# Kernel tuning notes

Measured on AMD Instinct MI355X. Metric: run time of the kernel, lower is better.

The kernel has to match this reference:

```python
import jax, jax.numpy as jnp
import numpy as np

THRESH = 0.1          # affinity threshold from init_kwargs
SCALES = (1, 2, 4, 8, 16)  # dyadic diffusion scales 2^0..2^4


def compute_dist(X):
    # X: [N, d] -> squared-euclidean pairwise distances via Gram matrix
    G = X @ X.T
    dg = jnp.diag(G)
    return dg[None, :] + dg[:, None] - 2.0 * G


def _diffuse(P, F):
    # returns [P^1 F, P^2 F, P^4 F, P^8 F, P^16 F] via 16 sequential applies
    outs = []
    cur = F
    for step in range(1, SCALES[-1] + 1):
        cur = P @ cur
        if step in SCALES:
            outs.append(cur)
    return outs


def _wavelet_bank(P, F):
    # lazy diffusion wavelets: psi_0 = I - P, psi_j = P^{2^{j-1}} - P^{2^j}
    lows = [F] + _diffuse(P, F)            # t = 0,1,2,4,8,16
    psis = [lows[j] - lows[j + 1] for j in range(len(lows) - 1)]  # 5 wavelets
    return psis, lows[-1]                  # (wavelet coeffs, low-pass P^16 F)


def _gwt_features(X):
    # X: [N, d] reweighted point cloud -> [N, 16*d] scattering features
    N, d = X.shape
    W = jnp.exp(-compute_dist(X) / 10.0)
    W = jnp.where(W < THRESH, jnp.zeros_like(W), W)   # sparsify affinity
    deg = W.sum(axis=1, keepdims=True)                # self-loop w=1 => deg>=1
    P = 0.5 * (jnp.eye(N, dtype=X.dtype) + W / deg)   # lazy random walk
    psis, low = _wavelet_bank(P, X)
    firsts = [jnp.abs(p) for p in psis]
    U = jnp.concatenate(firsts, axis=1)               # [N, 5*d] diffuse all at once
    psis2, _ = _wavelet_bank(P, U)
    # second order: |psi_{j2} |psi_{j1} x|| only for j2 > j1 (10 pairs)
    seconds = [jnp.abs(psis2[j2][:, : j2 * d]) for j2 in range(1, len(psis2))]
    return jnp.concatenate([low] + firsts + seconds, axis=1)  # [N, (1+5+10)*d]


def setup_inputs() -> dict:
    key = jax.random.key(0)
    k1, k2 = jax.random.split(key)
    point_clouds = jax.random.normal(k1, (4, 2048, 3), dtype=jnp.float32)
    alphas = jax.random.uniform(k2, (4, 3), dtype=jnp.float32)  # learned param
    return {"point_clouds": point_clouds, "alphas": alphas}


def reference(point_clouds, alphas):
    # point_clouds: [B, N, d]; alphas: [K, d]
    Xb = point_clouds[:, None, :, :] * alphas[None, :, None, :]  # [B, K, N, d]
    feats = jax.vmap(jax.vmap(_gwt_features))(Xb)                # [B, K, N, 16d]
    # per-cloud: cat over K along feature dim then mean over nodes == mean then flatten
    return feats.mean(axis=2).reshape(feats.shape[0], -1)        # [B, K*16*d]
```

## Files before the change

kernel.cpp:

```cpp
#include <hip/hip_runtime.h>
#include <hip/hip_bf16.h>


#define NN 2048
#define NPAIR 16

typedef _Float16 half8 __attribute__((ext_vector_type(8)));
typedef _Float16 f16x2 __attribute__((ext_vector_type(2)));
typedef float f32x4 __attribute__((ext_vector_type(4)));

extern "C" __device__ f16x2 __ocml_exp2_2f16(f16x2);

#define C2F 0.28853900817779268f
#define CWF -0.14426950408889634f
#define NL2T 3.3219280948873623f

template<int MODE>
__global__ __launch_bounds__(512, 8)
void apply_k(const float* __restrict__ pc, const float* __restrict__ alphas,
             float* __restrict__ Xs, _Float16* __restrict__ Xp,
             float* __restrict__ ihd,
             const _Float16* __restrict__ cur, _Float16* __restrict__ out,
             float* __restrict__ lvl, int t,
             const float* __restrict__ LT1u, const float* __restrict__ LT2r,
             float* __restrict__ fout) {
    __shared__ __align__(16) float smem[8576];
    const int tid  = threadIdx.x;
    const int lane = tid & 63;
    const int wv   = tid >> 6;
    const int p    = blockIdx.y;
    const int m0   = blockIdx.x * 32;
    const int idx16 = lane & 15, quad = lane >> 4;
    const int b = p >> 2;

    float a0, a1, a2;
    if (MODE == 0) {
        const int kk = p & 3;
        a0 = alphas[kk * 3 + 0]; a1 = alphas[kk * 3 + 1]; a2 = alphas[kk * 3 + 2];
        if (blockIdx.x == 0 && tid < 48) fout[p * 48 + tid] = 0.f;
        float4* dst = (float4*)smem;
#pragma unroll
        for (int e = 0; e < 2; ++e) {
            const int idx = wv * 128 + e * 64 + lane;
            const float* r = pc + ((size_t)b * NN + idx * 2) * 3;
            float x0 = r[0] * a0, y0 = r[1] * a1, z0 = r[2] * a2;
            float x1 = r[3] * a0, y1 = r[4] * a1, z1 = r[5] * a2;
            float q0 = CWF * (x0 * x0 + y0 * y0 + z0 * z0);
            float q1 = CWF * (x1 * x1 + y1 * y1 + z1 * z1);
            union { float4 f; f16x2 h[4]; } ev;
            ev.h[0] = (f16x2){(_Float16)x0, (_Float16)x1};
            ev.h[1] = (f16x2){(_Float16)y0, (_Float16)y1};
            ev.h[2] = (f16x2){(_Float16)z0, (_Float16)z1};
            ev.h[3] = (f16x2){(_Float16)q0, (_Float16)q1};
            dst[idx] = ev.f;
            if (blockIdx.x == 0) ((float4*)Xp)[(size_t)p * 1024 + idx] = ev.f;
        }
    } else {
        const float4* src = (const float4*)(Xp + (size_t)p * 8192);
        float4* dst = (float4*)smem;
        dst[wv * 128 + lane]      = src[wv * 128 + lane];
        dst[wv * 128 + 64 + lane] = src[wv * 128 + 64 + lane];
    }

    f16x2 qi2[2], xx2[2], xy2[2], xz2[2];
#pragma unroll
    for (int s = 0; s < 2; ++s) {
        const int row = m0 + s * 16 + idx16;
        float fx, fy, fz, fq;
        if (MODE == 0) {
            const float* r = pc + ((size_t)b * NN + row) * 3;
            fx = r[0] * a0; fy = r[1] * a1; fz = r[2] * a2;
            fq = CWF * (fx * fx + fy * fy + fz * fz);
            if (wv == 0 && quad == 0) {
                float4 o; o.x = fx; o.y = fy; o.z = fz; o.w = fq;
                *(float4*)(Xs + ((size_t)p * NN + row) * 4) = o;
            }
        } else {
            float4 v = *(const float4*)(Xs + ((size_t)p * NN + row) * 4);
            fx = v.x; fy = v.y; fz = v.z; fq = v.w;
        }
        _Float16 q = (_Float16)(fq + NL2T);
        _Float16 x = (_Float16)(C2F * fx);
        _Float16 y = (_Float16)(C2F * fy);
        _Float16 z = (_Float16)(C2F * fz);
        qi2[s] = (f16x2){q, q}; xx2[s] = (f16x2){x, x};
        xy2[s] = (f16x2){y, y}; xz2[s] = (f16x2){z, z};
    }
    const f16x2 SC2 = (f16x2){(_Float16)32768.f, (_Float16)32768.f};
    const f16x2 ONE2 = (f16x2){(_Float16)1.f, (_Float16)1.f};
    const f16x2 ZER2 = (f16x2){(_Float16)0.f, (_Float16)0.f};

    const _Float16* bp = cur + ((size_t)p * 16 + idx16) * NN + wv * 256 + quad * 8;
    f32x4 acc[2] = {{0.f,0.f,0.f,0.f},{0.f,0.f,0.f,0.f}};

    for (int kc = 0; kc < 8; ++kc) {
        const int pb = wv * 128 + kc * 16 + quad * 4;
        union { f16x2 h2[4]; half8 h8; } bfu;
        if (MODE != 0) {
            bool ld;
            if (MODE == 3)                 ld = true;
            else if (MODE == 1 || MODE == 2) ld = (idx16 < 3);
            else if (MODE == 4)            ld = (idx16 >= 3);
            else                           ld = (idx16 >= 4);
            if (ld) bfu.h8 = *(const half8*)(bp + kc * 32);
            else {
#pragma unroll
                for (int z = 0; z < 4; ++z) bfu.h2[z] = ZER2;
            }
        }
        union { f16x2 h2[4]; half8 h8; } af[2];
#pragma unroll
        for (int jp = 0; jp < 4; ++jp) {
            union { float4 f; f16x2 h[4]; } e;
            e.f = ((const float4*)smem)[pb + jp];
            if (MODE == 0) {
                bfu.h2[jp] = (idx16 == 0) ? e.h[0]
                           : (idx16 == 1) ? e.h[1]
                           : (idx16 == 2) ? e.h[2]
                           : (idx16 == 3) ? ONE2 : ZER2;
            }
#pragma unroll
            for (int s = 0; s < 2; ++s) {
                f16x2 tv = qi2[s] + e.h[3];
                tv = __builtin_elementwise_fma(xx2[s], e.h[0], tv);
                tv = __builtin_elementwise_fma(xy2[s], e.h[1], tv);
                tv = __builtin_elementwise_fma(xz2[s], e.h[2], tv);
                f16x2 u = __builtin_elementwise_min(tv, tv * SC2);
                af[s].h2[jp] = __ocml_exp2_2f16(u);
            }
        }
#pragma unroll
        for (int s = 0; s < 2; ++s)
            acc[s] = __builtin_amdgcn_mfma_f32_16x16x32_f16(af[s].h8, bfu.h8, acc[s], 0, 0, 0);
    }

    const int n  = tid >> 5;
    const int rr = tid & 31;
    const int s2 = rr >> 4, mloc = rr & 15;
    const int base = s2 * 256 + (mloc >> 2) * 64 + (mloc & 3);
    const int row = m0 + rr;
    float ihEff;
    if (MODE != 0) ihEff = 0.1f * ihd[p * NN + row];

#pragma unroll
    for (int s = 0; s < 2; ++s)
        *(f32x4*)&smem[4096 + wv * 512 + s * 256 + lane * 4] = acc[s];
    __syncthreads();

    float sum = 0.f;
#pragma unroll
    for (int g = 0; g < 8; ++g) sum += smem[4096 + g * 512 + base + n * 4];
    if (MODE == 0) {
        float deg10 = 0.f;
#pragma unroll
        for (int g = 0; g < 8; ++g) deg10 += smem[4096 + g * 512 + base + 12];
        float ih = 5.0f / deg10;
        if (n == 3) ihd[p * NN + row] = ih;
        ihEff = 0.1f * ih;
    }
    float cv;
    if (MODE == 0) {
        cv = (n < 3) ? pc[((size_t)b * NN + row) * 3 + n] * alphas[(p & 3) * 3 + n] : 0.f;
    } else if (MODE == 1 || MODE == 2) {
        cv = (n < 3) ? (float)cur[((size_t)p * 16 + n) * NN + row] : 0.f;
    } else if (MODE == 3) {
        cv = (float)cur[((size_t)p * 16 + n) * NN + row];
    } else {
        cv = (n >= 4) ? (float)cur[((size_t)p * 16 + n) * NN + row] : 0.f;
    }
    float o1v = 0.5f * cv + ihEff * sum;

    if (MODE == 0 || MODE == 1) {
        if (n < 3) {
            out[((size_t)p * 16 + n) * NN + row] = (_Float16)o1v;
            if (lvl) lvl[(((size_t)p * 5 + t) * 16 + n) * NN + row] = o1v;
        }
    } else if (MODE == 2) {
        if (n < 3) {
            lvl[(((size_t)p * 5 + t) * 16 + n) * NN + row] = o1v;
            smem[8192 + n * 32 + rr] = o1v;
        }
        __syncthreads();
        float oval = o1v;
        if (n >= 4) {
            const int u = n - 4, jw = u / 3, c = u - 3 * jw;
            float a = (jw == 0) ? Xs[((size_t)p * NN + row) * 4 + c]
                                : LT1u[(((size_t)p * 5 + (jw - 1)) * 16 + c) * NN + row];
            float bb = (jw == 3) ? smem[8192 + c * 32 + rr]
                                 : LT1u[(((size_t)p * 5 + jw) * 16 + c) * NN + row];
            oval = fabsf(a - bb);
        }
        out[((size_t)p * 16 + n) * NN + row] = (_Float16)oval;
    } else if (MODE == 3) {
        out[((size_t)p * 16 + n) * NN + row] = (_Float16)o1v;
        if (lvl && (n >= 4 || (t == 3 && n < 3)))
            lvl[(((size_t)p * 5 + t) * 16 + n) * NN + row] = o1v;
    } else if (MODE == 4) {
        if (n >= 4) out[((size_t)p * 16 + n) * NN + row] = (_Float16)o1v;
    } else {
        if (n >= 4) smem[8192 + (n - 4) * 32 + rr] = o1v;
        __syncthreads();
        if (tid < 384) {
            const int f = tid >> 3, g = tid & 7;
            const float* l1 = LT1u + (size_t)p * 5 * 16 * NN;
            const float* l2 = LT2r + (size_t)p * 5 * 16 * NN;
            float s = 0.f;
#pragma unroll
            for (int k = 0; k < 4; ++k) {
                const int m = m0 + g * 4 + k;
                float v;
                if (f < 3) {
                    v = l2[((size_t)3 * 16 + f) * NN + m];
                } else if (f < 18) {
                    int j = (f - 3) / 3, c = (f - 3) % 3;
                    float a = (j == 0) ? Xs[((size_t)p * NN + m) * 4 + c]
                                       : l1[((size_t)(j - 1) * 16 + c) * NN + m];
                    float bb = (j < 4) ? l1[((size_t)j * 16 + c) * NN + m]
                                       : l2[((size_t)3 * 16 + c) * NN + m];
                    v = fabsf(a - bb);
                } else {
                    int gg = f - 18, j2, uc;
                    if (gg < 3)       { j2 = 1; uc = gg; }
                    else if (gg < 9)  { j2 = 2; uc = gg - 3; }
                    else if (gg < 18) { j2 = 3; uc = gg - 9; }
                    else              { j2 = 4; uc = gg - 18; }
                    float a = l2[((size_t)(j2 - 1) * 16 + uc + 4) * NN + m];
                    float bb = (j2 == 4) ? smem[8192 + uc * 32 + (g * 4 + k)]
                                         : l2[((size_t)j2 * 16 + uc + 4) * NN + m];
                    v = fabsf(a - bb);
                }
                s += v;
            }
#pragma unroll
            for (int off = 4; off > 0; off >>= 1) s += __shfl_down(s, off, 8);
            if (g == 0) atomicAdd(&fout[p * 48 + f], s * (1.0f / NN));
        }
    }
}

extern "C" void kernel_launch(void* const* d_in, const int* in_sizes, int n_in,
                              void* d_out, int out_size, void* d_ws, size_t ws_size,
                              hipStream_t stream) {
    const float* pc     = (const float*)d_in[0];
    const float* alphas = (const float*)d_in[1];
    float* outp = (float*)d_out;

    char* base = (char*)d_ws;
    size_t off = 0;
    auto carve = [&](size_t bytes) -> void* {
        void* r = base + off;
        off = (off + bytes + 255) & ~(size_t)255;
        return r;
    };
    float*     Xs  = (float*)carve((size_t)NPAIR * NN * 4 * sizeof(float));
    _Float16*  Xp  = (_Float16*)carve((size_t)NPAIR * 1024 * 8 * 2);
    float*     ihd = (float*)carve((size_t)NPAIR * NN * sizeof(float));
    _Float16*  pA  = (_Float16*)carve((size_t)NPAIR * 16 * NN * 2);
    _Float16*  pB  = (_Float16*)carve((size_t)NPAIR * 16 * NN * 2);
    float*     LT1 = (float*)carve((size_t)NPAIR * 5 * 16 * NN * sizeof(float));
    float*     LT2 = (float*)carve((size_t)NPAIR * 5 * 16 * NN * sizeof(float));

    dim3 gridA(NN / 32, NPAIR);

    apply_k<0><<<gridA, 512, 0, stream>>>(pc, alphas, Xs, Xp, ihd,
        nullptr, pA, LT1, 0, nullptr, nullptr, outp);
    const _Float16* c1 = pA;
    int slot = 1;

    for (int step = 2; step <= 8; ++step) {
        _Float16* o1 = (c1 == pA) ? pB : pA;
        bool sv = (step & (step - 1)) == 0;
        if (step == 8)
            apply_k<2><<<gridA, 512, 0, stream>>>(pc, alphas, Xs, Xp, ihd,
                c1, o1, LT1, 3, LT1, nullptr, nullptr);
        else
            apply_k<1><<<gridA, 512, 0, stream>>>(pc, alphas, Xs, Xp, ihd,
                c1, o1, sv ? LT1 : nullptr, slot, nullptr, nullptr, nullptr);
        if (sv) ++slot;
        c1 = o1;
    }

    int slot2 = 0;
    for (int i = 1; i <= 16; ++i) {
        _Float16* o1 = (c1 == pA) ? pB : pA;
        if (i == 16) {
            apply_k<5><<<gridA, 512, 0, stream>>>(pc, alphas, Xs, Xp, ihd,
                c1, o1, nullptr, 4, LT1, LT2, outp);
        } else if (i <= 8) {
            bool sv = (i & (i - 1)) == 0;
            apply_k<3><<<gridA, 512, 0, stream>>>(pc, alphas, Xs, Xp, ihd,
                c1, o1, sv ? LT2 : nullptr, slot2, nullptr, nullptr, nullptr);
            if (sv) ++slot2;
        } else {
            apply_k<4><<<gridA, 512, 0, stream>>>(pc, alphas, Xs, Xp, ihd,
                c1, o1, nullptr, 0, nullptr, nullptr, nullptr);
        }
        c1 = o1;
    }
}
```

Baseline: 423.3 us.

## Shrink apply blocks to 16 rows with 4 waves and vectorized epilogue

Each apply block now covers 16 output rows with 256 threads (4 waves splitting K into 512-wide chunks) instead of 32 rows with 512 threads, doubling grid size. Cross-wave reduction is done by wave 0 summing three partial MFMA tiles from shared memory. Wave 0 then writes four consecutive rows per lane with half4/float4 stores, and the degree is taken via a shuffle. This raises block count and cuts shared memory per block, aiming at better occupancy and fewer epilogue transactions. The cost is that the affinity matrix is recomputed per row-tile: each block rebuilds its 16×2048 exp tile, and the redundant per-block Xp staging load doubles in total.

```diff
diff --git a/kernel.cpp b/kernel.cpp
--- a/kernel.cpp
+++ b/kernel.cpp
@@ -6,6 +6,7 @@
 #define NPAIR 16
 
 typedef _Float16 half8 __attribute__((ext_vector_type(8)));
+typedef _Float16 half4 __attribute__((ext_vector_type(4)));
 typedef _Float16 f16x2 __attribute__((ext_vector_type(2)));
 typedef float f32x4 __attribute__((ext_vector_type(4)));
 
@@ -16,7 +17,7 @@
 #define NL2T 3.3219280948873623f
 
 template<int MODE>
-__global__ __launch_bounds__(512, 8)
+__global__ __launch_bounds__(256, 8)
 void apply_k(const float* __restrict__ pc, const float* __restrict__ alphas,
              float* __restrict__ Xs, _Float16* __restrict__ Xp,
              float* __restrict__ ihd,
@@ -24,12 +25,12 @@
              float* __restrict__ lvl, int t,
              const float* __restrict__ LT1u, const float* __restrict__ LT2r,
              float* __restrict__ fout) {
-    __shared__ __align__(16) float smem[8576];
+    __shared__ __align__(16) float smem[4864];
     const int tid  = threadIdx.x;
     const int lane = tid & 63;
     const int wv   = tid >> 6;
     const int p    = blockIdx.y;
-    const int m0   = blockIdx.x * 32;
+    const int m0   = blockIdx.x * 16;
     const int idx16 = lane & 15, quad = lane >> 4;
     const int b = p >> 2;
 
@@ -40,8 +41,8 @@
         if (blockIdx.x == 0 && tid < 48) fout[p * 48 + tid] = 0.f;
         float4* dst = (float4*)smem;
 #pragma unroll
-        for (int e = 0; e < 2; ++e) {
-            const int idx = wv * 128 + e * 64 + lane;
+        for (int e = 0; e < 4; ++e) {
+            const int idx = wv * 256 + e * 64 + lane;
             const float* r = pc + ((size_t)b * NN + idx * 2) * 3;
             float x0 = r[0] * a0, y0 = r[1] * a1, z0 = r[2] * a2;
             float x1 = r[3] * a0, y1 = r[4] * a1, z1 = r[5] * a2;
@@ -58,14 +59,14 @@
     } else {
         const float4* src = (const float4*)(Xp + (size_t)p * 8192);
         float4* dst = (float4*)smem;
-        dst[wv * 128 + lane]      = src[wv * 128 + lane];
-        dst[wv * 128 + 64 + lane] = src[wv * 128 + 64 + lane];
-    }
-
-    f16x2 qi2[2], xx2[2], xy2[2], xz2[2];
-#pragma unroll
-    for (int s = 0; s < 2; ++s) {
-        const int row = m0 + s * 16 + idx16;
+#pragma unroll
+        for (int e = 0; e < 4; ++e)
+            dst[wv * 256 + e * 64 + lane] = src[wv * 256 + e * 64 + lane];
+    }
+
+    f16x2 qi2, xx2, xy2, xz2;
+    {
+        const int row = m0 + idx16;
         float fx, fy, fz, fq;
         if (MODE == 0) {
             const float* r = pc + ((size_t)b * NN + row) * 3;
@@ -83,32 +84,31 @@
         _Float16 x = (_Float16)(C2F * fx);
         _Float16 y = (_Float16)(C2F * fy);
         _Float16 z = (_Float16)(C2F * fz);
-        qi2[s] = (f16x2){q, q}; xx2[s] = (f16x2){x, x};
-        xy2[s] = (f16x2){y, y}; xz2[s] = (f16x2){z, z};
-    }
-    const f16x2 SC2 = (f16x2){(_Float16)32768.f, (_Float16)32768.f};
+        qi2 = (f16x2){q, q}; xx2 = (f16x2){x, x};
+        xy2 = (f16x2){y, y}; xz2 = (f16x2){z, z};
+    }
+    const f16x2 SC2  = (f16x2){(_Float16)32768.f, (_Float16)32768.f};
     const f16x2 ONE2 = (f16x2){(_Float16)1.f, (_Float16)1.f};
     const f16x2 ZER2 = (f16x2){(_Float16)0.f, (_Float16)0.f};
 
-    const _Float16* bp = cur + ((size_t)p * 16 + idx16) * NN + wv * 256 + quad * 8;
-    f32x4 acc[2] = {{0.f,0.f,0.f,0.f},{0.f,0.f,0.f,0.f}};
-
-    for (int kc = 0; kc < 8; ++kc) {
-        const int pb = wv * 128 + kc * 16 + quad * 4;
+    const _Float16* bp = cur + ((size_t)p * 16 + idx16) * NN + wv * 512 + quad * 8;
+    f32x4 acc = {0.f, 0.f, 0.f, 0.f};
+
+    for (int kc = 0; kc < 16; ++kc) {
+        const int pb = wv * 256 + kc * 16 + quad * 4;
         union { f16x2 h2[4]; half8 h8; } bfu;
         if (MODE != 0) {
             bool ld;
-            if (MODE == 3)                 ld = true;
+            if (MODE == 3)                   ld = true;
             else if (MODE == 1 || MODE == 2) ld = (idx16 < 3);
-            else if (MODE == 4)            ld = (idx16 >= 3);
-            else                           ld = (idx16 >= 4);
+            else                             ld = (idx16 >= 4);
             if (ld) bfu.h8 = *(const half8*)(bp + kc * 32);
             else {
 #pragma unroll
                 for (int z = 0; z < 4; ++z) bfu.h2[z] = ZER2;
             }
         }
-        union { f16x2 h2[4]; half8 h8; } af[2];
+        union { f16x2 h2[4]; half8 h8; } af;
 #pragma unroll
         for (int jp = 0; jp < 4; ++jp) {
             union { float4 f; f16x2 h[4]; } e;
@@ -119,89 +119,140 @@
                            : (idx16 == 2) ? e.h[2]
                            : (idx16 == 3) ? ONE2 : ZER2;
             }
-#pragma unroll
-            for (int s = 0; s < 2; ++s) {
-                f16x2 tv = qi2[s] + e.h[3];
-                tv = __builtin_elementwise_fma(xx2[s], e.h[0], tv);
-                tv = __builtin_elementwise_fma(xy2[s], e.h[1], tv);
-                tv = __builtin_elementwise_fma(xz2[s], e.h[2], tv);
-                f16x2 u = __builtin_elementwise_min(tv, tv * SC2);
-                af[s].h2[jp] = __ocml_exp2_2f16(u);
-            }
-        }
-#pragma unroll
-        for (int s = 0; s < 2; ++s)
-            acc[s] = __builtin_amdgcn_mfma_f32_16x16x32_f16(af[s].h8, bfu.h8, acc[s], 0, 0, 0);
-    }
-
-    const int n  = tid >> 5;
-    const int rr = tid & 31;
-    const int s2 = rr >> 4, mloc = rr & 15;
-    const int base = s2 * 256 + (mloc >> 2) * 64 + (mloc & 3);
-    const int row = m0 + rr;
-    float ihEff;
-    if (MODE != 0) ihEff = 0.1f * ihd[p * NN + row];
-
-#pragma unroll
-    for (int s = 0; s < 2; ++s)
-        *(f32x4*)&smem[4096 + wv * 512 + s * 256 + lane * 4] = acc[s];
+            f16x2 tv = qi2 + e.h[3];
+            tv = __builtin_elementwise_fma(xx2, e.h[0], tv);
+            tv = __builtin_elementwise_fma(xy2, e.h[1], tv);
+            tv = __builtin_elementwise_fma(xz2, e.h[2], tv);
+            f16x2 u = __builtin_elementwise_min(tv, tv * SC2);
+            af.h2[jp] = __ocml_exp2_2f16(u);
+        }
+        acc = __builtin_amdgcn_mfma_f32_16x16x32_f16(af.h8, bfu.h8, acc, 0, 0, 0);
+    }
+
+    if (wv != 0)
+        *(f32x4*)&smem[4096 + (wv - 1) * 256 + lane * 4] = acc;
     __syncthreads();
 
-    float sum = 0.f;
-#pragma unroll
-    for (int g = 0; g < 8; ++g) sum += smem[4096 + g * 512 + base + n * 4];
-    if (MODE == 0) {
-        float deg10 = 0.f;
-#pragma unroll
-        for (int g = 0; g < 8; ++g) deg10 += smem[4096 + g * 512 + base + 12];
-        float ih = 5.0f / deg10;
-        if (n == 3) ihd[p * NN + row] = ih;
-        ihEff = 0.1f * ih;
-    }
-    float cv;
-    if (MODE == 0) {
-        cv = (n < 3) ? pc[((size_t)b * NN + row) * 3 + n] * alphas[(p & 3) * 3 + n] : 0.f;
-    } else if (MODE == 1 || MODE == 2) {
-        cv = (n < 3) ? (float)cur[((size_t)p * 16 + n) * NN + row] : 0.f;
+    const int n  = idx16;
+    const int r0 = m0 + quad * 4;
+    float o1v[4], ihq[4];
+    if (wv == 0) {
+#pragma unroll
+        for (int g = 0; g < 3; ++g)
+            acc += *(const f32x4*)&smem[4096 + g * 256 + lane * 4];
+        if (MODE == 0) {
+#pragma unroll
+            for (int j = 0; j < 4; ++j) {
+                float deg10 = __shfl(acc[j], quad * 16 + 3, 64);
+                ihq[j] = 5.0f / deg10;
+            }
+            if (n == 3) {
+                float4 iv; iv.x = ihq[0]; iv.y = ihq[1]; iv.z = ihq[2]; iv.w = ihq[3];
+                *(float4*)(ihd + (size_t)p * NN + r0) = iv;
+            }
+        } else {
+            float4 iv = *(const float4*)(ihd + (size_t)p * NN + r0);
+            ihq[0] = iv.x; ihq[1] = iv.y; ihq[2] = iv.z; ihq[3] = iv.w;
+        }
+        float cv[4];
+        if (MODE == 0) {
+#pragma unroll
+            for (int j = 0; j < 4; ++j)
+                cv[j] = (n < 3) ? pc[((size_t)b * NN + r0 + j) * 3 + n]
+                                  * (n == 0 ? a0 : (n == 1 ? a1 : a2))
+                                : 0.f;
+        } else {
+            half4 cvv = *(const half4*)(cur + ((size_t)p * 16 + n) * NN + r0);
+#pragma unroll
+            for (int j = 0; j < 4; ++j) {
+                bool live;
+                if (MODE == 1 || MODE == 2) live = (n < 3);
+                else if (MODE == 3)         live = true;
+                else                        live = (n >= 4);
+                cv[j] = live ? (float)cvv[j] : 0.f;
+            }
+        }
+#pragma unroll
+        for (int j = 0; j < 4; ++j)
+            o1v[j] = 0.5f * cv[j] + 0.1f * ihq[j] * acc[j];
+    }
+
+    if (MODE == 0 || MODE == 1) {
+        if (wv != 0) return;
+        if (n < 3) {
+            half4 ov = {(_Float16)o1v[0], (_Float16)o1v[1],
+                        (_Float16)o1v[2], (_Float16)o1v[3]};
+            *(half4*)(out + ((size_t)p * 16 + n) * NN + r0) = ov;
+            if (lvl) {
+                float4 lv; lv.x = o1v[0]; lv.y = o1v[1]; lv.z = o1v[2]; lv.w = o1v[3];
+                *(float4*)(lvl + (((size_t)p * 5 + t) * 16 + n) * NN + r0) = lv;
+            }
+        }
+        return;
     } else if (MODE == 3) {
-        cv = (float)cur[((size_t)p * 16 + n) * NN + row];
-    } else {
-        cv = (n >= 4) ? (float)cur[((size_t)p * 16 + n) * NN + row] : 0.f;
-    }
-    float o1v = 0.5f * cv + ihEff * sum;
-
-    if (MODE == 0 || MODE == 1) {
-        if (n < 3) {
-            out[((size_t)p * 16 + n) * NN + row] = (_Float16)o1v;
-            if (lvl) lvl[(((size_t)p * 5 + t) * 16 + n) * NN + row] = o1v;
-        }
+        if (wv != 0) return;
+        half4 ov = {(_Float16)o1v[0], (_Float16)o1v[1],
+                    (_Float16)o1v[2], (_Float16)o1v[3]};
+        *(half4*)(out + ((size_t)p * 16 + n) * NN + r0) = ov;
+        if (lvl && (n >= 4 || (t == 3 && n < 3))) {
+            float4 lv; lv.x = o1v[0]; lv.y = o1v[1]; lv.z = o1v[2]; lv.w = o1v[3];
+            *(float4*)(lvl + (((size_t)p * 5 + t) * 16 + n) * NN + r0) = lv;
+        }
+        return;
+    } else if (MODE == 4) {
+        if (wv != 0) return;
+        if (n >= 4) {
+            half4 ov = {(_Float16)o1v[0], (_Float16)o1v[1],
+                        (_Float16)o1v[2], (_Float16)o1v[3]};
+            *(half4*)(out + ((size_t)p * 16 + n) * NN + r0) = ov;
+        }
+        return;
     } else if (MODE == 2) {
-        if (n < 3) {
-            lvl[(((size_t)p * 5 + t) * 16 + n) * NN + row] = o1v;
-            smem[8192 + n * 32 + rr] = o1v;
+        if (wv == 0 && n < 3) {
+            float4 lv; lv.x = o1v[0]; lv.y = o1v[1]; lv.z = o1v[2]; lv.w = o1v[3];
+            *(float4*)(lvl + (((size_t)p * 5 + t) * 16 + n) * NN + r0) = lv;
+#pragma unroll
+            for (int j = 0; j < 4; ++j) smem[4096 + n * 16 + quad * 4 + j] = o1v[j];
         }
         __syncthreads();
-        float oval = o1v;
+        if (wv != 0) return;
+        float ov[4];
+#pragma unroll
+        for (int j = 0; j < 4; ++j) ov[j] = o1v[j];
         if (n >= 4) {
             const int u = n - 4, jw = u / 3, c = u - 3 * jw;
-            float a = (jw == 0) ? Xs[((size_t)p * NN + row) * 4 + c]
-                                : LT1u[(((size_t)p * 5 + (jw - 1)) * 16 + c) * NN + row];
-            float bb = (jw == 3) ? smem[8192 + c * 32 + rr]
-                                 : LT1u[(((size_t)p * 5 + jw) * 16 + c) * NN + row];
-            oval = fabsf(a - bb);
-        }
-        out[((size_t)p * 16 + n) * NN + row] = (_Float16)oval;
-    } else if (MODE == 3) {
-        out[((size_t)p * 16 + n) * NN + row] = (_Float16)o1v;
-        if (lvl && (n >= 4 || (t == 3 && n < 3)))
-            lvl[(((size_t)p * 5 + t) * 16 + n) * NN + row] = o1v;
-    } else if (MODE == 4) {
-        if (n >= 4) out[((size_t)p * 16 + n) * NN + row] = (_Float16)o1v;
+            float av[4], bv[4];
+            if (jw == 0) {
+#pragma unroll
+                for (int j = 0; j < 4; ++j)
+                    av[j] = Xs[((size_t)p * NN + r0 + j) * 4 + c];
+            } else {
+                float4 t4 = *(const float4*)(LT1u + (((size_t)p * 5 + (jw - 1)) * 16 + c) * NN + r0);
+                av[0] = t4.x; av[1] = t4.y; av[2] = t4.z; av[3] = t4.w;
+            }
+            if (jw == 3) {
+#pragma unroll
+                for (int j = 0; j < 4; ++j)
+                    bv[j] = smem[4096 + c * 16 + quad * 4 + j];
+            } else {
+                float4 t4 = *(const float4*)(LT1u + (((size_t)p * 5 + jw) * 16 + c) * NN + r0);
+                bv[0] = t4.x; bv[1] = t4.y; bv[2] = t4.z; bv[3] = t4.w;
+            }
+#pragma unroll
+            for (int j = 0; j < 4; ++j) ov[j] = fabsf(av[j] - bv[j]);
+        }
+        half4 o = {(_Float16)ov[0], (_Float16)ov[1], (_Float16)ov[2], (_Float16)ov[3]};
+        *(half4*)(out + ((size_t)p * 16 + n) * NN + r0) = o;
+        return;
     } else {
-        if (n >= 4) smem[8192 + (n - 4) * 32 + rr] = o1v;
+        if (wv == 0 && n >= 4) {
+#pragma unroll
+            for (int j = 0; j < 4; ++j)
+                smem[4096 + (n - 4) * 16 + quad * 4 + j] = o1v[j];
+        }
         __syncthreads();
-        if (tid < 384) {
-            const int f = tid >> 3, g = tid & 7;
+        if (tid < 192) {
+            const int f = tid >> 2, g = tid & 3;
             const float* l1 = LT1u + (size_t)p * 5 * 16 * NN;
             const float* l2 = LT2r + (size_t)p * 5 * 16 * NN;
             float s = 0.f;
@@ -225,16 +276,17 @@
                     else if (gg < 18) { j2 = 3; uc = gg - 9; }
                     else              { j2 = 4; uc = gg - 18; }
                     float a = l2[((size_t)(j2 - 1) * 16 + uc + 4) * NN + m];
-                    float bb = (j2 == 4) ? smem[8192 + uc * 32 + (g * 4 + k)]
+                    float bb = (j2 == 4) ? smem[4096 + uc * 16 + (g * 4 + k)]
                                          : l2[((size_t)j2 * 16 + uc + 4) * NN + m];
                     v = fabsf(a - bb);
                 }
                 s += v;
             }
 #pragma unroll
-            for (int off = 4; off > 0; off >>= 1) s += __shfl_down(s, off, 8);
+            for (int off = 2; off > 0; off >>= 1) s += __shfl_down(s, off, 4);
             if (g == 0) atomicAdd(&fout[p * 48 + f], s * (1.0f / NN));
         }
+        return;
     }
 }
 
@@ -260,9 +312,9 @@
     float*     LT1 = (float*)carve((size_t)NPAIR * 5 * 16 * NN * sizeof(float));
     float*     LT2 = (float*)carve((size_t)NPAIR * 5 * 16 * NN * sizeof(float));
 
-    dim3 gridA(NN / 32, NPAIR);
-
-    apply_k<0><<<gridA, 512, 0, stream>>>(pc, alphas, Xs, Xp, ihd,
+    dim3 gridA(NN / 16, NPAIR);
+
+    apply_k<0><<<gridA, 256, 0, stream>>>(pc, alphas, Xs, Xp, ihd,
         nullptr, pA, LT1, 0, nullptr, nullptr, outp);
     const _Float16* c1 = pA;
     int slot = 1;
@@ -271,10 +323,10 @@
         _Float16* o1 = (c1 == pA) ? pB : pA;
         bool sv = (step & (step - 1)) == 0;
         if (step == 8)
-            apply_k<2><<<gridA, 512, 0, stream>>>(pc, alphas, Xs, Xp, ihd,
+            apply_k<2><<<gridA, 256, 0, stream>>>(pc, alphas, Xs, Xp, ihd,
                 c1, o1, LT1, 3, LT1, nullptr, nullptr);
         else
-            apply_k<1><<<gridA, 512, 0, stream>>>(pc, alphas, Xs, Xp, ihd,
+            apply_k<1><<<gridA, 256, 0, stream>>>(pc, alphas, Xs, Xp, ihd,
                 c1, o1, sv ? LT1 : nullptr, slot, nullptr, nullptr, nullptr);
         if (sv) ++slot;
         c1 = o1;
@@ -284,15 +336,15 @@
     for (int i = 1; i <= 16; ++i) {
         _Float16* o1 = (c1 == pA) ? pB : pA;
         if (i == 16) {
-            apply_k<5><<<gridA, 512, 0, stream>>>(pc, alphas, Xs, Xp, ihd,
+            apply_k<5><<<gridA, 256, 0, stream>>>(pc, alphas, Xs, Xp, ihd,
                 c1, o1, nullptr, 4, LT1, LT2, outp);
         } else if (i <= 8) {
             bool sv = (i & (i - 1)) == 0;
-            apply_k<3><<<gridA, 512, 0, stream>>>(pc, alphas, Xs, Xp, ihd,
+            apply_k<3><<<gridA, 256, 0, stream>>>(pc, alphas, Xs, Xp, ihd,
                 c1, o1, sv ? LT2 : nullptr, slot2, nullptr, nullptr, nullptr);
             if (sv) ++slot2;
         } else {
-            apply_k<4><<<gridA, 512, 0, stream>>>(pc, alphas, Xs, Xp, ihd,
+            apply_k<4><<<gridA, 256, 0, stream>>>(pc, alphas, Xs, Xp, ihd,
                 c1, o1, nullptr, 0, nullptr, nullptr, nullptr);
         }
         c1 = o1;
```

After: 478.7 us. 13.1% more time.
